# Optimization experiments

Measured on AMD Instinct MI355X. Metric: run time of the kernel, lower is better.

Reference implementation:

```python
import jax, jax.numpy as jnp
import numpy as np

COMMITMENT_COST = 0.25
NUM_EMBEDDINGS = 1024
EMBEDDING_DIM = 256


def setup_inputs() -> dict:
    key = jax.random.key(0)
    k1, k2 = jax.random.split(key)
    inputs = jax.random.normal(k1, (64, 256, 32, 32), dtype=jnp.float32)
    emb_w = jax.random.normal(k2, (NUM_EMBEDDINGS, EMBEDDING_DIM), dtype=jnp.float32)
    return {"inputs": inputs, "emb_w": emb_w}


def reference(inputs, emb_w):
    # NCHW -> NHWC, flatten to [N, D]
    x = jnp.transpose(inputs, (0, 2, 3, 1))  # [B, H, W, D]
    B, H, W, D = x.shape
    flat = x.reshape(-1, D)  # [N, D]

    distances = (
        jnp.sum(flat * flat, axis=1, keepdims=True)
        + jnp.sum(emb_w * emb_w, axis=1)
        - 2.0 * flat @ emb_w.T
    )
    idx = jnp.argmin(distances, axis=1)  # [N]

    # one-hot @ W is just a gather of codebook rows
    quantized = emb_w[idx].reshape(B, H, W, D)

    # avg_probs = mean of one-hot encodings = normalized codeword counts
    counts = jnp.zeros((NUM_EMBEDDINGS,), dtype=jnp.float32).at[idx].add(1.0)
    avg_probs = counts / flat.shape[0]
    perplexity = jnp.exp(-jnp.sum(avg_probs * jnp.log(avg_probs + 1e-10)))

    e_latent_loss = jnp.mean((jax.lax.stop_gradient(quantized) - x) ** 2)
    loss = COMMITMENT_COST * e_latent_loss

    # straight-through estimator
    quantized_st = x + jax.lax.stop_gradient(quantized - x)
    quantized_out = jnp.transpose(quantized_st, (0, 3, 1, 2))  # back to NCHW

    return loss, quantized_out, perplexity, idx.reshape(B, H, W)
```

## Files before the change

### kernel.cpp

```cpp
#include <hip/hip_runtime.h>
#include <hip/hip_bf16.h>
#include <math.h>

typedef _Float16 f16;
typedef __attribute__((ext_vector_type(8))) _Float16 f16x8;
typedef __attribute__((ext_vector_type(16))) float f32x16;
typedef float4 float4_u __attribute__((aligned(4)));

#define DIMS 256
#define NCODE 1024
#define NPTS 65536

#define OUT_Q_OFF 1
#define OUT_PERP_OFF 16777217
#define OUT_IDX_OFF 16777218

#define EHI_F32_OFF 4
#define ELO_F32_OFF (4 + 131072)
#define TILE_BYTES 16384

#define XSTRIDE 132

__device__ __forceinline__ void gload_lds16(const void* g, void* l) {
    __builtin_amdgcn_global_load_lds(
        (const __attribute__((address_space(1))) unsigned int*)g,
        (__attribute__((address_space(3))) unsigned int*)l, 16, 0, 0);
}

__global__ __launch_bounds__(256) void k_eprep(const float* __restrict__ ew,
                                               char* __restrict__ ehi,
                                               char* __restrict__ elo,
                                               float* __restrict__ enorm) {
    int w = threadIdx.x >> 6;
    int l = threadIdx.x & 63;
    int row = blockIdx.x * 4 + w;
    float4 v = *reinterpret_cast<const float4*>(ew + (size_t)row * DIMS + l * 4);
    float vv[4] = {v.x, v.y, v.z, v.w};
    __align__(8) f16 hh[4];
    __align__(8) f16 ll[4];
    float s = 0.0f;
    #pragma unroll
    for (int e = 0; e < 4; ++e) {
        f16 h = (f16)vv[e];
        hh[e] = h;
        ll[e] = (f16)(vv[e] - (float)h);
        s += vv[e] * vv[e];
    }
    size_t off = (size_t)(row >> 5) * TILE_BYTES + (size_t)(row & 31) * 512
               + (size_t)((((l >> 1) ^ (row & 7)) << 4) + ((l & 1) << 3));
    *reinterpret_cast<float2*>(ehi + off) = *reinterpret_cast<float2*>(hh);
    *reinterpret_cast<float2*>(elo + off) = *reinterpret_cast<float2*>(ll);
    #pragma unroll
    for (int off2 = 32; off2 > 0; off2 >>= 1) s += __shfl_down(s, off2);
    if (l == 0) enorm[row] = s;
}

__global__ __launch_bounds__(512, 1) void k_argmin_mfma(const float* __restrict__ x,
                                                        const char* __restrict__ ehi,
                                                        const char* __restrict__ elo,
                                                        const float* __restrict__ enorm,
                                                        int* __restrict__ out_idx) {
    __shared__ __align__(16) char smem[3 * 2 * TILE_BYTES];
    __shared__ float enorm_lds[NCODE];
    float* Xs = (float*)smem;

    const int t = threadIdx.x;
    const int wave = t >> 6;
    const int lane = t & 63;
    const int lrow = lane & 31;
    const int lhalf = lane >> 5;

    const int blk = blockIdx.x;
    const int b = blk >> 2;
    const int hw0 = (blk & 3) << 8;
    const float* xb = x + (size_t)b * (DIMS * 1024) + hw0;

    enorm_lds[t] = enorm[t];
    enorm_lds[t + 512] = enorm[t + 512];

    f16x8 ahi[16], alo[16];
    #pragma unroll
    for (int dc = 0; dc < 4; ++dc) {
        #pragma unroll
        for (int h = 0; h < 2; ++h) {
            __syncthreads();
            #pragma unroll
            for (int i = 0; i < 4; ++i) {
                int id = i * 512 + t;
                int d = id >> 5;
                int p4 = id & 31;
                float4 v = *reinterpret_cast<const float4*>(
                    xb + (size_t)(dc * 64 + d) * 1024 + h * 128 + p4 * 4);
                *reinterpret_cast<float4*>(&Xs[d * XSTRIDE + p4 * 4]) = v;
            }
            __syncthreads();
            if ((wave >> 2) == h) {
                int p = (wave & 3) * 32 + lrow;
                #pragma unroll
                for (int kcl = 0; kcl < 4; ++kcl) {
                    f16x8 hh, ll;
                    #pragma unroll
                    for (int e = 0; e < 8; ++e) {
                        float xv = Xs[(kcl * 16 + lhalf * 8 + e) * XSTRIDE + p];
                        f16 hi = (f16)xv;
                        hh[e] = hi;
                        ll[e] = (f16)(xv - (float)hi);
                    }
                    ahi[dc * 4 + kcl] = hh;
                    alo[dc * 4 + kcl] = ll;
                }
            }
        }
    }
    __syncthreads();

    const int plane = wave >> 2;
    const char* gplane = plane ? elo : ehi;
    const int pl_off = plane * TILE_BYTES;
    const int woff = (wave & 3) * 4096;

    #pragma unroll
    for (int k = 0; k < 2; ++k) {
        #pragma unroll
        for (int i = 0; i < 4; ++i) {
            int off = woff + i * 1024;
            gload_lds16(gplane + (size_t)k * TILE_BYTES + off + lane * 16,
                        smem + k * (2 * TILE_BYTES) + pl_off + off);
        }
    }
    asm volatile("s_waitcnt vmcnt(4)" ::: "memory");
    __builtin_amdgcn_s_barrier();

    float bestv[16];
    int besti[16];
    #pragma unroll
    for (int r = 0; r < 16; ++r) { bestv[r] = -3.4e38f; besti[r] = 0; }

#define ROUND_BODY(ACC_CUR, ACC_PREV, RD)                                         \
    {                                                                             \
        const int rd_ = (RD);                                                     \
        const int cur_ = rd_ % 3;                                                 \
        if (rd_ + 2 < 32) {                                                       \
            const int nx_ = (rd_ + 2) % 3;                                        \
            const char* gp_ = gplane + (size_t)(rd_ + 2) * TILE_BYTES;            \
            char* lp_ = smem + nx_ * (2 * TILE_BYTES) + pl_off;                   \
            _Pragma("unroll")                                                     \
            for (int i_ = 0; i_ < 4; ++i_) {                                      \
                int off_ = woff + i_ * 1024;                                      \
                gload_lds16(gp_ + off_ + lane * 16, lp_ + off_);                  \
            }                                                                     \
        }                                                                         \
        const char* EHb_ = smem + cur_ * (2 * TILE_BYTES);                        \
        const char* ELb_ = EHb_ + TILE_BYTES;                                     \
        float nh_ = -0.5f * enorm_lds[rd_ * 32 + lrow];                           \
        _Pragma("unroll")                                                         \
        for (int r_ = 0; r_ < 16; ++r_) ACC_CUR[r_] = nh_;                        \
        __builtin_amdgcn_s_setprio(1);                                            \
        _Pragma("unroll")                                                         \
        for (int kc_ = 0; kc_ < 16; ++kc_) {                                      \
            int g_ = kc_ * 2 + lhalf;                                             \
            int ra_ = lrow * 512 + ((g_ ^ (lrow & 7)) << 4);                      \
            f16x8 bh_ = *reinterpret_cast<const f16x8*>(EHb_ + ra_);              \
            f16x8 bl_ = *reinterpret_cast<const f16x8*>(ELb_ + ra_);              \
            ACC_CUR = __builtin_amdgcn_mfma_f32_32x32x16_f16(ahi[kc_], bh_, ACC_CUR, 0, 0, 0); \
            ACC_CUR = __builtin_amdgcn_mfma_f32_32x32x16_f16(ahi[kc_], bl_, ACC_CUR, 0, 0, 0); \
            ACC_CUR = __builtin_amdgcn_mfma_f32_32x32x16_f16(alo[kc_], bh_, ACC_CUR, 0, 0, 0); \
        }                                                                         \
        __builtin_amdgcn_s_setprio(0);                                            \
        if (rd_ > 0) {                                                            \
            const int cw_ = (rd_ - 1) * 32 + lrow;                                \
            _Pragma("unroll")                                                     \
            for (int r_ = 0; r_ < 16; ++r_) {                                     \
                float s_ = ACC_PREV[r_];                                          \
                if (s_ > bestv[r_]) { bestv[r_] = s_; besti[r_] = cw_; }          \
            }                                                                     \
        }                                                                         \
             \
                     \
        if (rd_ + 2 < 32) asm volatile("s_waitcnt vmcnt(4)" ::: "memory");        \
        else              asm volatile("s_waitcnt vmcnt(0)" ::: "memory");        \
        __builtin_amdgcn_s_barrier();                                             \
    }

    f32x16 accA, accB;
    for (int rr = 0; rr < 16; ++rr) {
        ROUND_BODY(accA, accB, 2 * rr);
        ROUND_BODY(accB, accA, 2 * rr + 1);
    }
    {
        int cw = 31 * 32 + lrow;
        #pragma unroll
        for (int r = 0; r < 16; ++r) {
            float s = accB[r];
            if (s > bestv[r]) { bestv[r] = s; besti[r] = cw; }
        }
    }
#undef ROUND_BODY

    #pragma unroll
    for (int off = 1; off <= 16; off <<= 1) {
        #pragma unroll
        for (int r = 0; r < 16; ++r) {
            float ov = __shfl_xor(bestv[r], off);
            int oi = __shfl_xor(besti[r], off);
            if (ov > bestv[r] || (ov == bestv[r] && oi < besti[r])) {
                bestv[r] = ov;
                besti[r] = oi;
            }
        }
    }
    if (lrow == 0) {
        #pragma unroll
        for (int r = 0; r < 16; ++r) {
            int row = (r & 3) + 8 * (r >> 2) + 4 * lhalf;
            out_idx[blk * 256 + wave * 32 + row] = besti[r];
        }
    }
}

#define QSTRIDE 258
__global__ __launch_bounds__(512) void k_quant(const float* __restrict__ x,
                                               const float* __restrict__ ew,
                                               const int* __restrict__ idxv,
                                               float* __restrict__ out,
                                               float* __restrict__ loss_acc,
                                               int* __restrict__ counts) {
    __shared__ float Eq[64 * QSTRIDE];
    __shared__ int ids[64];
    __shared__ int h[NCODE];
    const int t = threadIdx.x;
    const int blk = blockIdx.x;
    const int b = blk >> 4;
    const int hw0 = (blk & 15) << 6;

    if (t < 64) ids[t] = idxv[(b << 10) + hw0 + t];
    h[t] = 0;
    if (t < 512) h[t + 512] = 0;
    __syncthreads();

    if (t < 64) atomicAdd(&h[ids[t]], 1);

    #pragma unroll
    for (int i = 0; i < 8; ++i) {
        int f = i * 512 + t;
        int row = f >> 6;
        int c4 = f & 63;
        float4 v = *reinterpret_cast<const float4*>(ew + (size_t)ids[row] * DIMS + c4 * 4);
        float2 lo2 = {v.x, v.y};
        float2 hi2 = {v.z, v.w};
        *reinterpret_cast<float2*>(&Eq[row * QSTRIDE + c4 * 4]) = lo2;
        *reinterpret_cast<float2*>(&Eq[row * QSTRIDE + c4 * 4 + 2]) = hi2;
    }
    __syncthreads();

    const int q4 = t & 15;
    const int cb = t >> 4;
    const int p = q4 * 4;
    float lsum = 0.0f;
    #pragma unroll
    for (int k = 0; k < 8; ++k) {
        int c = k * 32 + cb;
        unsigned g = ((unsigned)b << 18) | ((unsigned)c << 10) | (unsigned)(hw0 + p);
        float4 xv = *reinterpret_cast<const float4*>(x + g);
        float q0 = Eq[(p + 0) * QSTRIDE + c];
        float q1 = Eq[(p + 1) * QSTRIDE + c];
        float q2 = Eq[(p + 2) * QSTRIDE + c];
        float q3 = Eq[(p + 3) * QSTRIDE + c];
        float d0 = q0 - xv.x, d1 = q1 - xv.y, d2 = q2 - xv.z, d3 = q3 - xv.w;
        float4 o;
        o.x = xv.x + d0; o.y = xv.y + d1; o.z = xv.z + d2; o.w = xv.w + d3;
        *reinterpret_cast<float4_u*>(out + OUT_Q_OFF + g) = o;
        lsum += d0 * d0 + d1 * d1 + d2 * d2 + d3 * d3;
    }
    #pragma unroll
    for (int off = 32; off > 0; off >>= 1) lsum += __shfl_down(lsum, off);
    if ((t & 63) == 0) atomicAdd(&loss_acc[blk & 63], lsum);

    int v0 = h[t];
    if (v0) atomicAdd(&counts[t], v0);
    if (t < 512) {
        int v1 = h[t + 512];
        if (v1) atomicAdd(&counts[t + 512], v1);
    }
    if (t < 64) out[OUT_IDX_OFF + (b << 10) + hw0 + t] = (float)ids[t];
}

__global__ __launch_bounds__(256) void k_final(const int* __restrict__ counts,
                                               const float* __restrict__ loss_acc,
                                               float* __restrict__ out) {
    int t = threadIdx.x;
    float s = 0.0f;
    #pragma unroll
    for (int i = 0; i < 4; ++i) {
        int cnt = counts[t + 256 * i];
        float p = (float)cnt * (1.0f / 65536.0f);
        s += p * logf(p + 1e-10f);
    }
    #pragma unroll
    for (int off = 32; off > 0; off >>= 1) s += __shfl_down(s, off);
    __shared__ float wsum[4];
    if ((t & 63) == 0) wsum[t >> 6] = s;
    __syncthreads();
    if (t == 0) {
        float S = wsum[0] + wsum[1] + wsum[2] + wsum[3];
        out[OUT_PERP_OFF] = expf(-S);
        float ls = 0.0f;
        for (int i = 0; i < 64; ++i) ls += loss_acc[i];
        out[0] = 0.25f * (ls * (1.0f / 16777216.0f));
    }
}

extern "C" void kernel_launch(void* const* d_in, const int* in_sizes, int n_in,
                              void* d_out, int out_size, void* d_ws, size_t ws_size,
                              hipStream_t stream) {
    const float* x = (const float*)d_in[0];
    const float* ew = (const float*)d_in[1];
    float* out = (float*)d_out;
    float* ws = (float*)d_ws;

    float* loss_acc = ws;
    int* counts = (int*)(ws + 64);
    float* enorm = ws + 64 + 1024;
    int* idxv = (int*)(ws + 64 + 2048);

    char* ehi = (char*)(out + EHI_F32_OFF);
    char* elo = (char*)(out + ELO_F32_OFF);

    hipMemsetAsync(d_ws, 0, (64 + 1024) * sizeof(float), stream);

    k_eprep<<<256, 256, 0, stream>>>(ew, ehi, elo, enorm);
    k_argmin_mfma<<<256, 512, 0, stream>>>(x, ehi, elo, enorm, idxv);
    k_quant<<<1024, 512, 0, stream>>>(x, ew, idxv, out, loss_acc, counts);
    k_final<<<1, 256, 0, stream>>>(counts, loss_acc, out);
}
```

Before: 166.9 us.

## Process 64-codeword tiles with double buffering and two interleaved accumulators

Codebook tiles grow from 32 to 64 codewords, and the codebook prep layout is changed to match. The argmin loop now runs 16 rounds with two independent MFMA accumulator chains interleaved, in place of 32 rounds with a triple-buffered, software-pipelined compare of the previous accumulator. This halves the number of barriers and gives the MFMA unit two independent dependency chains. In exchange it drops from triple to double buffering, uses a full __syncthreads with an implicit vmcnt(0) wait each round, and compares results right after the MFMAs rather than overlapping that work with the next round.

```diff
diff --git a/kernel.cpp b/kernel.cpp
--- a/kernel.cpp
+++ b/kernel.cpp
@@ -17,7 +17,8 @@
 
 #define EHI_F32_OFF 4
 #define ELO_F32_OFF (4 + 131072)
-#define TILE_BYTES 16384
+#define TILE2 32768
+#define BUFB 65536
 
 #define XSTRIDE 132
 
@@ -46,7 +47,7 @@
         ll[e] = (f16)(vv[e] - (float)h);
         s += vv[e] * vv[e];
     }
-    size_t off = (size_t)(row >> 5) * TILE_BYTES + (size_t)(row & 31) * 512
+    size_t off = (size_t)(row >> 6) * TILE2 + (size_t)(row & 63) * 512
                + (size_t)((((l >> 1) ^ (row & 7)) << 4) + ((l & 1) << 3));
     *reinterpret_cast<float2*>(ehi + off) = *reinterpret_cast<float2*>(hh);
     *reinterpret_cast<float2*>(elo + off) = *reinterpret_cast<float2*>(ll);
@@ -60,7 +61,7 @@
                                                         const char* __restrict__ elo,
                                                         const float* __restrict__ enorm,
                                                         int* __restrict__ out_idx) {
-    __shared__ __align__(16) char smem[3 * 2 * TILE_BYTES];
+    __shared__ __align__(16) char smem[2 * BUFB];
     __shared__ float enorm_lds[NCODE];
     float* Xs = (float*)smem;
 
@@ -116,86 +117,71 @@
 
     const int plane = wave >> 2;
     const char* gplane = plane ? elo : ehi;
-    const int pl_off = plane * TILE_BYTES;
-    const int woff = (wave & 3) * 4096;
-
-    #pragma unroll
-    for (int k = 0; k < 2; ++k) {
-        #pragma unroll
-        for (int i = 0; i < 4; ++i) {
-            int off = woff + i * 1024;
-            gload_lds16(gplane + (size_t)k * TILE_BYTES + off + lane * 16,
-                        smem + k * (2 * TILE_BYTES) + pl_off + off);
-        }
-    }
-    asm volatile("s_waitcnt vmcnt(4)" ::: "memory");
-    __builtin_amdgcn_s_barrier();
+    const int pl_off = plane * TILE2;
+    const int woff = (wave & 3) * 8192;
+
+    #pragma unroll
+    for (int i = 0; i < 8; ++i) {
+        int off = woff + i * 1024;
+        gload_lds16(gplane + off + lane * 16, smem + pl_off + off);
+    }
+    __syncthreads();
 
     float bestv[16];
     int besti[16];
     #pragma unroll
     for (int r = 0; r < 16; ++r) { bestv[r] = -3.4e38f; besti[r] = 0; }
 
-#define ROUND_BODY(ACC_CUR, ACC_PREV, RD)                                         \
-    {                                                                             \
-        const int rd_ = (RD);                                                     \
-        const int cur_ = rd_ % 3;                                                 \
-        if (rd_ + 2 < 32) {                                                       \
-            const int nx_ = (rd_ + 2) % 3;                                        \
-            const char* gp_ = gplane + (size_t)(rd_ + 2) * TILE_BYTES;            \
-            char* lp_ = smem + nx_ * (2 * TILE_BYTES) + pl_off;                   \
-            _Pragma("unroll")                                                     \
-            for (int i_ = 0; i_ < 4; ++i_) {                                      \
-                int off_ = woff + i_ * 1024;                                      \
-                gload_lds16(gp_ + off_ + lane * 16, lp_ + off_);                  \
-            }                                                                     \
-        }                                                                         \
-        const char* EHb_ = smem + cur_ * (2 * TILE_BYTES);                        \
-        const char* ELb_ = EHb_ + TILE_BYTES;                                     \
-        float nh_ = -0.5f * enorm_lds[rd_ * 32 + lrow];                           \
-        _Pragma("unroll")                                                         \
-        for (int r_ = 0; r_ < 16; ++r_) ACC_CUR[r_] = nh_;                        \
-        __builtin_amdgcn_s_setprio(1);                                            \
-        _Pragma("unroll")                                                         \
-        for (int kc_ = 0; kc_ < 16; ++kc_) {                                      \
-            int g_ = kc_ * 2 + lhalf;                                             \
-            int ra_ = lrow * 512 + ((g_ ^ (lrow & 7)) << 4);                      \
-            f16x8 bh_ = *reinterpret_cast<const f16x8*>(EHb_ + ra_);              \
-            f16x8 bl_ = *reinterpret_cast<const f16x8*>(ELb_ + ra_);              \
-            ACC_CUR = __builtin_amdgcn_mfma_f32_32x32x16_f16(ahi[kc_], bh_, ACC_CUR, 0, 0, 0); \
-            ACC_CUR = __builtin_amdgcn_mfma_f32_32x32x16_f16(ahi[kc_], bl_, ACC_CUR, 0, 0, 0); \
-            ACC_CUR = __builtin_amdgcn_mfma_f32_32x32x16_f16(alo[kc_], bh_, ACC_CUR, 0, 0, 0); \
-        }                                                                         \
-        __builtin_amdgcn_s_setprio(0);                                            \
-        if (rd_ > 0) {                                                            \
-            const int cw_ = (rd_ - 1) * 32 + lrow;                                \
-            _Pragma("unroll")                                                     \
-            for (int r_ = 0; r_ < 16; ++r_) {                                     \
-                float s_ = ACC_PREV[r_];                                          \
-                if (s_ > bestv[r_]) { bestv[r_] = s_; besti[r_] = cw_; }          \
-            }                                                                     \
-        }                                                                         \
-             \
-                     \
-        if (rd_ + 2 < 32) asm volatile("s_waitcnt vmcnt(4)" ::: "memory");        \
-        else              asm volatile("s_waitcnt vmcnt(0)" ::: "memory");        \
-        __builtin_amdgcn_s_barrier();                                             \
-    }
-
-    f32x16 accA, accB;
-    for (int rr = 0; rr < 16; ++rr) {
-        ROUND_BODY(accA, accB, 2 * rr);
-        ROUND_BODY(accB, accA, 2 * rr + 1);
-    }
-    {
-        int cw = 31 * 32 + lrow;
-        #pragma unroll
-        for (int r = 0; r < 16; ++r) {
-            float s = accB[r];
-            if (s > bestv[r]) { bestv[r] = s; besti[r] = cw; }
-        }
-    }
-#undef ROUND_BODY
+    for (int rd = 0; rd < 16; ++rd) {
+        if (rd + 1 < 16) {
+            const char* gp = gplane + (size_t)(rd + 1) * TILE2;
+            char* lp = smem + ((rd + 1) & 1) * BUFB + pl_off;
+            #pragma unroll
+            for (int i = 0; i < 8; ++i) {
+                int off = woff + i * 1024;
+                gload_lds16(gp + off + lane * 16, lp + off);
+            }
+        }
+
+        const char* EHb = smem + (rd & 1) * BUFB;
+        const char* ELb = EHb + TILE2;
+        f32x16 acc0, acc1;
+        float nh0 = -0.5f * enorm_lds[rd * 64 + lrow];
+        float nh1 = -0.5f * enorm_lds[rd * 64 + 32 + lrow];
+        #pragma unroll
+        for (int r = 0; r < 16; ++r) { acc0[r] = nh0; acc1[r] = nh1; }
+
+        __builtin_amdgcn_s_setprio(1);
+        #pragma unroll
+        for (int kc = 0; kc < 16; ++kc) {
+            int g = kc * 2 + lhalf;
+            int ra = lrow * 512 + ((g ^ (lrow & 7)) << 4);
+            f16x8 bh0 = *reinterpret_cast<const f16x8*>(EHb + ra);
+            f16x8 bh1 = *reinterpret_cast<const f16x8*>(EHb + ra + 16384);
+            f16x8 bl0 = *reinterpret_cast<const f16x8*>(ELb + ra);
+            f16x8 bl1 = *reinterpret_cast<const f16x8*>(ELb + ra + 16384);
+            acc0 = __builtin_amdgcn_mfma_f32_32x32x16_f16(ahi[kc], bh0, acc0, 0, 0, 0);
+            acc1 = __builtin_amdgcn_mfma_f32_32x32x16_f16(ahi[kc], bh1, acc1, 0, 0, 0);
+            acc0 = __builtin_amdgcn_mfma_f32_32x32x16_f16(ahi[kc], bl0, acc0, 0, 0, 0);
+            acc1 = __builtin_amdgcn_mfma_f32_32x32x16_f16(ahi[kc], bl1, acc1, 0, 0, 0);
+            acc0 = __builtin_amdgcn_mfma_f32_32x32x16_f16(alo[kc], bh0, acc0, 0, 0, 0);
+            acc1 = __builtin_amdgcn_mfma_f32_32x32x16_f16(alo[kc], bh1, acc1, 0, 0, 0);
+        }
+        __builtin_amdgcn_s_setprio(0);
+
+        {
+            int cw0 = rd * 64 + lrow;
+            int cw1 = cw0 + 32;
+            #pragma unroll
+            for (int r = 0; r < 16; ++r) {
+                float s0 = acc0[r];
+                if (s0 > bestv[r]) { bestv[r] = s0; besti[r] = cw0; }
+                float s1 = acc1[r];
+                if (s1 > bestv[r]) { bestv[r] = s1; besti[r] = cw1; }
+            }
+        }
+        __syncthreads();
+    }
 
     #pragma unroll
     for (int off = 1; off <= 16; off <<= 1) {
```

New measurement: 162.9 us. 2.4% less time.
